# Kernel optimization log

Hardware: AMD Instinct MI355X
Metric: run time of the kernel (lower is better)

## Reference

```python
import jax, jax.numpy as jnp
import numpy as np
from jax.scipy.special import logsumexp

B, L, S, C = 8, 2048, 2048, 256
ITERS = 20

def setup_inputs() -> dict:
    key = jax.random.key(0)
    k0, k1 = jax.random.split(key)
    feat_c0 = jax.random.normal(k0, (B, L, C), dtype=jnp.float32)
    feat_c1 = jax.random.normal(k1, (B, S, C), dtype=jnp.float32)
    bin_score = jnp.ones((), dtype=jnp.float32)  # init_bin_score = 1.0
    return {"feat_c0": feat_c0, "feat_c1": feat_c1, "bin_score": bin_score}

def _uniform_prior(b, m, n):
    # build_uniform_prior: norm = -log(m+n); log_mu/[log_nu] over augmented rows/cols
    fm, fn = jnp.float32(m), jnp.float32(n)
    norm = -jnp.log(fm + fn)
    log_mu = jnp.concatenate([jnp.full((m,), norm, jnp.float32), (jnp.log(fn) + norm)[None]])
    log_nu = jnp.concatenate([jnp.full((n,), norm, jnp.float32), (jnp.log(fm) + norm)[None]])
    log_mu = jnp.broadcast_to(log_mu[None], (b, m + 1))
    log_nu = jnp.broadcast_to(log_nu[None], (b, n + 1))
    return log_mu, log_nu, norm

def _log_sinkhorn(Z, log_mu, log_nu, iters):
    u0 = jnp.zeros_like(log_mu)
    v0 = jnp.zeros_like(log_nu)
    def body(carry, _):
        u, v = carry
        u = log_mu - logsumexp(Z + v[:, None, :], axis=2)  # [B, M+1]
        v = log_nu - logsumexp(Z + u[:, :, None], axis=1)  # [B, N+1]
        return (u, v), None
    (u, v), _ = jax.lax.scan(body, (u0, v0), None, length=iters)
    return Z + u[:, :, None] + v[:, None, :]

def reference(feat_c0, feat_c1, bin_score):
    b, m, n = feat_c0.shape[0], feat_c0.shape[1], feat_c1.shape[1]
    scores = jnp.einsum('blc,bsc->bls', feat_c0, feat_c1)  # [B, M, N]
    # augment with dustbin row/col
    bins0 = jnp.broadcast_to(bin_score, (b, m, 1))
    bins1 = jnp.broadcast_to(bin_score, (b, 1, n))
    alpha = jnp.broadcast_to(bin_score, (b, 1, 1))
    Zin = jnp.concatenate([
        jnp.concatenate([scores, bins0], axis=-1),
        jnp.concatenate([bins1, alpha], axis=-1),
    ], axis=1)  # [B, M+1, N+1]
    log_mu, log_nu, norm = _uniform_prior(b, m, n)
    Z = _log_sinkhorn(Zin, log_mu, log_nu, ITERS)
    return Z - norm
```

## Files before the change

kernel.cpp:

```cpp
#include <hip/hip_runtime.h>

#define Bn 8
#define Mn 2048
#define Nn 2048
#define Cn 256
#define Np1 2049
#define Mp1 2049
#define UVS 2056
#define SINK_ITERS 20
#define NORM   (-8.3177661667193428f)
#define LOGBIN (-0.6931471805599453f)
#define LOG2E  (1.4426950408889634f)
#define LN2    (0.6931471805599453f)
#define NORM2  (-12.0f)
#define LOGBIN2 (-1.0f)
#define PNORM  (8.3177661667193428f)

#define EXP2(x) __builtin_amdgcn_exp2f(x)
#define LOG2(x) __builtin_amdgcn_logf(x)

typedef __bf16 v8bf __attribute__((ext_vector_type(8)));
typedef float  v4f  __attribute__((ext_vector_type(4)));
typedef unsigned short v8u __attribute__((ext_vector_type(8)));

__device__ __forceinline__ float bf2f(unsigned short h){
  return __uint_as_float(((unsigned)h) << 16);
}
__device__ __forceinline__ unsigned short f2bf(float f){
  unsigned u = __float_as_uint(f);
  return (unsigned short)((u + 0x7FFFu + ((u >> 16) & 1u)) >> 16);
}
__device__ __forceinline__ float ldS(const float* p){ return *p; }
__device__ __forceinline__ float ldS(const unsigned short* p){ return bf2f(*p); }
__device__ __forceinline__ void  stS(float* p, float x){ *p = x; }
__device__ __forceinline__ void  stS(unsigned short* p, float x){ *p = f2bf(x); }

__device__ __forceinline__ void ons(float x, float& m, float& s){
  if (x <= m) { s += __expf(x - m); }
  else        { s = s * __expf(m - x) + 1.0f; m = x; }
}
__device__ __forceinline__ void comb(float& m, float& s, float m2, float s2){
  if (m2 <= m) { s += s2 * __expf(m2 - m); }
  else         { s = s * __expf(m - m2) + s2; m = m2; }
}

__global__ void __launch_bounds__(256) conv_k(
    const float* __restrict__ in, unsigned short* __restrict__ out, float scale)
{
  size_t idx = (size_t)blockIdx.x * 256 + threadIdx.x;
  const float* p = in + idx * 8;
  v4f a = *(const v4f*)p;
  v4f c = *(const v4f*)(p + 4);
  v8u o;
  #pragma unroll
  for (int e = 0; e < 4; ++e){ o[e] = f2bf(a[e] * scale); o[e+4] = f2bf(c[e] * scale); }
  *(v8u*)(out + idx * 8) = o;
}

__global__ void __launch_bounds__(256) gemm_bt(
    const unsigned short* __restrict__ A, const unsigned short* __restrict__ Bm,
    unsigned short* __restrict__ S, unsigned short* __restrict__ ST)
{
  __shared__ unsigned short lt[4][64][65];
  int wid  = (blockIdx.x * 256 + threadIdx.x) >> 6;
  int w    = (threadIdx.x >> 6) & 3;
  int lane = threadIdx.x & 63;
  int b  = wid >> 10;
  int tt = wid & 1023;
  int i0 = (tt >> 5) << 6;
  int j0 = (tt & 31) << 6;
  int ln = lane & 15, qd = lane >> 4;
  const unsigned short* Ab = A  + (size_t)b * Mn * Cn;
  const unsigned short* Bb = Bm + (size_t)b * Nn * Cn;

  v4f acc[4][4];
  #pragma unroll
  for (int r = 0; r < 4; ++r)
    #pragma unroll
    for (int c = 0; c < 4; ++c)
      #pragma unroll
      for (int e = 0; e < 4; ++e) acc[r][c][e] = 0.0f;

  #pragma unroll
  for (int k0 = 0; k0 < Cn; k0 += 32){
    int kk = k0 + qd * 8;
    v8bf af[4], bfr[4];
    #pragma unroll
    for (int r = 0; r < 4; ++r)
      af[r] = *(const v8bf*)(const void*)(Ab + (size_t)(i0 + r*16 + ln) * Cn + kk);
    #pragma unroll
    for (int c = 0; c < 4; ++c)
      bfr[c] = *(const v8bf*)(const void*)(Bb + (size_t)(j0 + c*16 + ln) * Cn + kk);
    #pragma unroll
    for (int r = 0; r < 4; ++r)
      #pragma unroll
      for (int c = 0; c < 4; ++c)
        acc[r][c] = __builtin_amdgcn_mfma_f32_16x16x32_bf16(af[r], bfr[c], acc[r][c], 0, 0, 0);
  }

  unsigned short* Sb = S + (size_t)b * Mn * Nn;
  #pragma unroll
  for (int r = 0; r < 4; ++r){
    #pragma unroll
    for (int e = 0; e < 4; ++e){
      int lr = r*16 + qd*4 + e;
      #pragma unroll
      for (int c = 0; c < 4; ++c){
        unsigned short hv = f2bf(acc[r][c][e] * LOG2E);
        Sb[(size_t)(i0 + lr) * Nn + (j0 + c*16 + ln)] = hv;
        lt[w][lr][c*16 + ln] = hv;
      }
    }
  }
  unsigned short* Tb = ST + (size_t)b * Mn * Nn;
  #pragma unroll
  for (int r = 0; r < 4; ++r){
    #pragma unroll
    for (int e = 0; e < 4; ++e){
      int p = r*16 + qd*4 + e;
      #pragma unroll
      for (int c = 0; c < 4; ++c){
        int q = c*16 + ln;
        Tb[(size_t)(j0 + p) * Mn + (i0 + q)] = lt[w][q][p];
      }
    }
  }
}

__global__ void __launch_bounds__(256) rmax_k(
    const unsigned short* __restrict__ S, float* __restrict__ rmax)
{
  int b = blockIdx.y, lane = threadIdx.x & 63;
  int i = blockIdx.x * 4 + (threadIdx.x >> 6);
  const unsigned short* Sr = S + ((size_t)b * Mn + i) * Nn;
  float m = -3.0e38f;
  #pragma unroll
  for (int q = 0; q < 4; ++q){
    v8u sv = *(const v8u*)(Sr + q * 512 + lane * 8);
    #pragma unroll
    for (int c = 0; c < 8; ++c) m = fmaxf(m, bf2f(sv[c]));
  }
  #pragma unroll
  for (int off = 32; off > 0; off >>= 1) m = fmaxf(m, __shfl_xor(m, off));
  if (lane == 0) rmax[(size_t)b * UVS + i] = m;
}

__global__ void __launch_bounds__(256) pass4_k(
    const unsigned short* __restrict__ S, const float* __restrict__ vin,
    float* __restrict__ uout, const float* __restrict__ rmax,
    const float* __restrict__ binp)
{
  int b = blockIdx.y, t = threadIdx.x;
  const float* vb = vin + (size_t)b * UVS;
  __shared__ float red[8];
  if (blockIdx.x < Mn / 8){
    int lane = t & 63, wv = t >> 6;
    int i0 = blockIdx.x * 8 + wv * 2;
    v4f va[8];
    #pragma unroll
    for (int q = 0; q < 4; ++q){
      int j0 = q * 512 + lane * 8;
      va[2*q]   = *(const v4f*)(vb + j0);
      va[2*q+1] = *(const v4f*)(vb + j0 + 4);
    }
    float mv = va[0][0];
    #pragma unroll
    for (int h = 0; h < 8; ++h)
      #pragma unroll
      for (int e = 0; e < 4; ++e) mv = fmaxf(mv, va[h][e]);
    #pragma unroll
    for (int off = 32; off > 0; off >>= 1) mv = fmaxf(mv, __shfl_xor(mv, off));
    float bin2 = binp[0] * LOG2E;
    float vN  = vb[Nn];
    float bvn = bin2 + vN;
    float sh0 = fmaxf(rmax[(size_t)b * UVS + i0]     + mv, bvn);
    float sh1 = fmaxf(rmax[(size_t)b * UVS + i0 + 1] + mv, bvn);
    const unsigned short* Sr0 = S + ((size_t)b * Mn + i0) * Nn;
    const unsigned short* Sr1 = Sr0 + Nn;
    float a0=0.f,a1=0.f,a2=0.f,a3=0.f;
    float c0=0.f,c1=0.f,c2=0.f,c3=0.f;
    #pragma unroll
    for (int q = 0; q < 4; ++q){
      int j0 = q * 512 + lane * 8;
      v8u r0 = *(const v8u*)(Sr0 + j0);
      v8u r1 = *(const v8u*)(Sr1 + j0);
      a0 += EXP2(bf2f(r0[0]) + va[2*q][0]   - sh0);
      a1 += EXP2(bf2f(r0[1]) + va[2*q][1]   - sh0);
      a2 += EXP2(bf2f(r0[2]) + va[2*q][2]   - sh0);
      a3 += EXP2(bf2f(r0[3]) + va[2*q][3]   - sh0);
      c0 += EXP2(bf2f(r1[0]) + va[2*q][0]   - sh1);
      c1 += EXP2(bf2f(r1[1]) + va[2*q][1]   - sh1);
      c2 += EXP2(bf2f(r1[2]) + va[2*q][2]   - sh1);
      c3 += EXP2(bf2f(r1[3]) + va[2*q][3]   - sh1);
      a0 += EXP2(bf2f(r0[4]) + va[2*q+1][0] - sh0);
      a1 += EXP2(bf2f(r0[5]) + va[2*q+1][1] - sh0);
      a2 += EXP2(bf2f(r0[6]) + va[2*q+1][2] - sh0);
      a3 += EXP2(bf2f(r0[7]) + va[2*q+1][3] - sh0);
      c0 += EXP2(bf2f(r1[4]) + va[2*q+1][0] - sh1);
      c1 += EXP2(bf2f(r1[5]) + va[2*q+1][1] - sh1);
      c2 += EXP2(bf2f(r1[6]) + va[2*q+1][2] - sh1);
      c3 += EXP2(bf2f(r1[7]) + va[2*q+1][3] - sh1);
    }
    float sA = (a0 + a1) + (a2 + a3);
    float sB = (c0 + c1) + (c2 + c3);
    #pragma unroll
    for (int off = 32; off > 0; off >>= 1){
      sA += __shfl_xor(sA, off);
      sB += __shfl_xor(sB, off);
    }
    if (lane == 0){
      sA += EXP2(bvn - sh0);
      sB += EXP2(bvn - sh1);
      uout[(size_t)b * UVS + i0]     = NORM2 - (sh0 + LOG2(sA));
      uout[(size_t)b * UVS + i0 + 1] = NORM2 - (sh1 + LOG2(sB));
    }
  } else {
    float x[9];
    #pragma unroll
    for (int k = 0; k < 9; ++k){
      int j = t + k * 256;
      x[k] = (j <= Nn) ? vb[j] : -3.0e38f;
    }
    float m = x[0];
    #pragma unroll
    for (int k = 1; k < 9; ++k) m = fmaxf(m, x[k]);
    #pragma unroll
    for (int off = 32; off > 0; off >>= 1) m = fmaxf(m, __shfl_down(m, off));
    int w = t >> 6;
    if ((t & 63) == 0) red[w] = m;
    __syncthreads();
    float M = fmaxf(fmaxf(red[0], red[1]), fmaxf(red[2], red[3]));
    float s = 0.0f;
    #pragma unroll
    for (int k = 0; k < 9; ++k) s += EXP2(x[k] - M);
    #pragma unroll
    for (int off = 32; off > 0; off >>= 1) s += __shfl_down(s, off);
    __syncthreads();
    if ((t & 63) == 0) red[w] = s;
    __syncthreads();
    if (t == 0){
      float Ss = red[0] + red[1] + red[2] + red[3];
      float bin2 = binp[0] * LOG2E;
      uout[(size_t)b * UVS + Mn] = LOGBIN2 - (bin2 + M + LOG2(Ss));
    }
  }
}

__global__ void __launch_bounds__(256) final2_k(
    const unsigned short* __restrict__ S, float* __restrict__ out,
    const float* __restrict__ u, const float* __restrict__ v,
    const float* __restrict__ binp)
{
  int i = blockIdx.x, b = blockIdx.y, t = threadIdx.x;
  float bin2 = binp[0] * LOG2E;
  const float* vb = v + (size_t)b * UVS;
  float ui = u[(size_t)b * UVS + i];
  float* ob = out + ((size_t)b * Mp1 + i) * Np1;
  if (i < Mn){
    const unsigned short* Sr = S + ((size_t)b * Mn + i) * Nn;
    int j0 = t * 8;
    v8u sv = *(const v8u*)(Sr + j0);
    v4f va = *(const v4f*)(vb + j0);
    v4f vc = *(const v4f*)(vb + j0 + 4);
    #pragma unroll
    for (int c = 0; c < 4; ++c) ob[j0 + c]     = (bf2f(sv[c])   + ui + va[c]) * LN2 + PNORM;
    #pragma unroll
    for (int c = 0; c < 4; ++c) ob[j0 + 4 + c] = (bf2f(sv[c+4]) + ui + vc[c]) * LN2 + PNORM;
    if (t == 0) ob[Nn] = (bin2 + ui + vb[Nn]) * LN2 + PNORM;
  } else {
    for (int j = t; j <= Nn; j += 256) ob[j] = (bin2 + ui + vb[j]) * LN2 + PNORM;
  }
}

template<typename ST>
__global__ void __launch_bounds__(256) gemm_k(
    const float* __restrict__ A, const float* __restrict__ Bm,
    ST* __restrict__ S, long srow, long sbatch)
{
  int wid  = (blockIdx.x * 256 + threadIdx.x) >> 6;
  int lane = threadIdx.x & 63;
  int b  = wid >> 10;
  int tt = wid & 1023;
  int i0 = (tt >> 5) << 6;
  int j0 = (tt & 31) << 6;
  int ln = lane & 15, qd = lane >> 4;
  const float* Ab = A  + (size_t)b * Mn * Cn;
  const float* Bb = Bm + (size_t)b * Nn * Cn;

  v4f acc[4][4];
  #pragma unroll
  for (int r = 0; r < 4; ++r)
    #pragma unroll
    for (int c = 0; c < 4; ++c)
      #pragma unroll
      for (int e = 0; e < 4; ++e) acc[r][c][e] = 0.0f;

  #pragma unroll
  for (int k0 = 0; k0 < Cn; k0 += 32){
    int kk = k0 + qd * 8;
    v8bf af[4], bfr[4];
    #pragma unroll
    for (int r = 0; r < 4; ++r){
      const float* p = Ab + (size_t)(i0 + r*16 + ln) * Cn + kk;
      v4f lo = *(const v4f*)p, hi = *(const v4f*)(p + 4);
      #pragma unroll
      for (int e = 0; e < 4; ++e){ af[r][e] = (__bf16)lo[e]; af[r][e+4] = (__bf16)hi[e]; }
    }
    #pragma unroll
    for (int c = 0; c < 4; ++c){
      const float* p = Bb + (size_t)(j0 + c*16 + ln) * Cn + kk;
      v4f lo = *(const v4f*)p, hi = *(const v4f*)(p + 4);
      #pragma unroll
      for (int e = 0; e < 4; ++e){ bfr[c][e] = (__bf16)lo[e]; bfr[c][e+4] = (__bf16)hi[e]; }
    }
    #pragma unroll
    for (int r = 0; r < 4; ++r)
      #pragma unroll
      for (int c = 0; c < 4; ++c)
        acc[r][c] = __builtin_amdgcn_mfma_f32_16x16x32_bf16(af[r], bfr[c], acc[r][c], 0, 0, 0);
  }

  ST* Sb = S + (size_t)b * sbatch;
  #pragma unroll
  for (int r = 0; r < 4; ++r){
    #pragma unroll
    for (int e = 0; e < 4; ++e){
      int row = i0 + r*16 + qd*4 + e;
      #pragma unroll
      for (int c = 0; c < 4; ++c)
        stS(Sb + (size_t)row * srow + (j0 + c*16 + ln), acc[r][c][e]);
    }
  }
}

__global__ void __launch_bounds__(256) row_pass_t(
    const unsigned short* __restrict__ S, const float* __restrict__ vin,
    float* __restrict__ uout, const float* __restrict__ binp)
{
  int b = blockIdx.y, t = threadIdx.x;
  const float* vb = vin + (size_t)b * UVS;
  __shared__ float red[8];
  if (blockIdx.x < Mn / 4){
    int lane = t & 63;
    int i = blockIdx.x * 4 + (t >> 6);
    const unsigned short* Sr = S + ((size_t)b * Mn + i) * Nn;
    float x[32];
    #pragma unroll
    for (int q = 0; q < 4; ++q){
      int j0 = q * 512 + lane * 8;
      v8u sv = *(const v8u*)(Sr + j0);
      v4f va = *(const v4f*)(vb + j0);
      v4f vc = *(const v4f*)(vb + j0 + 4);
      #pragma unroll
      for (int c = 0; c < 4; ++c){
        x[q*8 + c]     = bf2f(sv[c])   + va[c];
        x[q*8 + 4 + c] = bf2f(sv[c+4]) + vc[c];
      }
    }
    float mx[16];
    #pragma unroll
    for (int k = 0; k < 16; ++k) mx[k] = fmaxf(x[2*k], x[2*k+1]);
    #pragma unroll
    for (int k = 0; k < 8; ++k) mx[k] = fmaxf(mx[k], mx[k+8]);
    #pragma unroll
    for (int k = 0; k < 4; ++k) mx[k] = fmaxf(mx[k], mx[k+4]);
    float m = fmaxf(fmaxf(mx[0], mx[1]), fmaxf(mx[2], mx[3]));
    #pragma unroll
    for (int off = 32; off > 0; off >>= 1) m = fmaxf(m, __shfl_xor(m, off));
    float s0 = 0.f, s1 = 0.f, s2 = 0.f, s3 = 0.f;
    #pragma unroll
    for (int k = 0; k < 8; ++k){
      s0 += __expf(x[4*k]     - m);
      s1 += __expf(x[4*k + 1] - m);
      s2 += __expf(x[4*k + 2] - m);
      s3 += __expf(x[4*k + 3] - m);
    }
    float s = (s0 + s1) + (s2 + s3);
    #pragma unroll
    for (int off = 32; off > 0; off >>= 1) s += __shfl_xor(s, off);
    if (lane == 0){
      float M = m, Ss = s;
      comb(M, Ss, binp[0] + vb[Nn], 1.0f);
      uout[(size_t)b * UVS + i] = NORM - (M + __logf(Ss));
    }
  } else {
    float x[9];
    #pragma unroll
    for (int k = 0; k < 9; ++k){
      int j = t + k * 256;
      x[k] = (j <= Nn) ? vb[j] : -3.0e38f;
    }
    float m = x[0];
    #pragma unroll
    for (int k = 1; k < 9; ++k) m = fmaxf(m, x[k]);
    #pragma unroll
    for (int off = 32; off > 0; off >>= 1) m = fmaxf(m, __shfl_down(m, off));
    int w = t >> 6;
    if ((t & 63) == 0) red[w] = m;
    __syncthreads();
    float M = fmaxf(fmaxf(red[0], red[1]), fmaxf(red[2], red[3]));
    float s = 0.0f;
    #pragma unroll
    for (int k = 0; k < 9; ++k) s += __expf(x[k] - M);
    #pragma unroll
    for (int off = 32; off > 0; off >>= 1) s += __shfl_down(s, off);
    __syncthreads();
    if ((t & 63) == 0) red[w] = s;
    __syncthreads();
    if (t == 0){
      float Ss = red[0] + red[1] + red[2] + red[3];
      uout[(size_t)b * UVS + Mn] = LOGBIN - (binp[0] + M + __logf(Ss));
    }
  }
}

__global__ void __launch_bounds__(256) row_pass_v(
    const unsigned short* __restrict__ S, const float* __restrict__ v,
    float* __restrict__ u, const float* __restrict__ binp)
{
  int i = blockIdx.x, b = blockIdx.y, t = threadIdx.x;
  const float* vb = v + (size_t)b * UVS;
  float x[9];
  int K;
  if (i < Mn){
    const unsigned short* Sr = S + ((size_t)b * Mn + i) * Nn;
    int j0 = t * 8;
    v8u sv = *(const v8u*)(Sr + j0);
    v4f va = *(const v4f*)(vb + j0);
    v4f vc = *(const v4f*)(vb + j0 + 4);
    #pragma unroll
    for (int c = 0; c < 4; ++c){ x[c] = bf2f(sv[c]) + va[c]; x[c+4] = bf2f(sv[c+4]) + vc[c]; }
    K = 8;
  } else {
    #pragma unroll
    for (int k = 0; k < 9; ++k){
      int j = t + k * 256;
      x[k] = (j <= Nn) ? vb[j] : -3.0e38f;
    }
    K = 9;
  }
  float m = x[0];
  #pragma unroll
  for (int k = 1; k < 9; ++k) if (k < K) m = fmaxf(m, x[k]);
  #pragma unroll
  for (int off = 32; off > 0; off >>= 1) m = fmaxf(m, __shfl_down(m, off));
  __shared__ float red[8];
  int w = t >> 6;
  if ((t & 63) == 0) red[w] = m;
  __syncthreads();
  float M = fmaxf(fmaxf(red[0], red[1]), fmaxf(red[2], red[3]));
  float s = 0.0f;
  #pragma unroll
  for (int k = 0; k < 9; ++k) if (k < K) s += __expf(x[k] - M);
  #pragma unroll
  for (int off = 32; off > 0; off >>= 1) s += __shfl_down(s, off);
  __syncthreads();
  if ((t & 63) == 0) red[w] = s;
  __syncthreads();
  if (t == 0){
    float Ss = red[0] + red[1] + red[2] + red[3];
    float bin = binp[0];
    if (i < Mn){
      comb(M, Ss, bin + vb[Nn], 1.0f);
      u[(size_t)b * UVS + i] = NORM - (M + __logf(Ss));
    } else {
      u[(size_t)b * UVS + Mn] = LOGBIN - (bin + M + __logf(Ss));
    }
  }
}

__global__ void __launch_bounds__(256) col_pass_v(
    const unsigned short* __restrict__ S, const float* __restrict__ u,
    float* __restrict__ v, const float* __restrict__ binp)
{
  int blk = blockIdx.x, b = blockIdx.y, t = threadIdx.x;
  const float* ub = u + (size_t)b * UVS;
  __shared__ float lm[32][65];
  __shared__ float ls[32][65];
  __shared__ float red[16];
  if (blk < Nn / 64){
    int tx = t & 7, ty = t >> 3;
    int j0 = blk * 64 + tx * 8;
    const unsigned short* Sb = S + (size_t)b * Mn * Nn;
    float m[8], s[8];
    #pragma unroll
    for (int c = 0; c < 8; ++c){ m[c] = -3.0e38f; s[c] = 0.0f; }
    for (int i = ty; i < Mn; i += 32){
      v8u sv = *(const v8u*)(Sb + (size_t)i * Nn + j0);
      float ui = ub[i];
      #pragma unroll
      for (int c = 0; c < 8; ++c){
        float x  = bf2f(sv[c]) + ui;
        float mn = fmaxf(m[c], x);
        s[c] = s[c] * __expf(m[c] - mn) + __expf(x - mn);
        m[c] = mn;
      }
    }
    #pragma unroll
    for (int c = 0; c < 8; ++c){ lm[ty][tx*8 + c] = m[c]; ls[ty][tx*8 + c] = s[c]; }
    __syncthreads();
    if (t < 64){
      float M = -3.0e38f, Ss = 0.0f;
      #pragma unroll 4
      for (int rg = 0; rg < 32; ++rg) comb(M, Ss, lm[rg][t], ls[rg][t]);
      float bin = binp[0];
      comb(M, Ss, bin + ub[Mn], 1.0f);
      v[(size_t)b * UVS + blk * 64 + t] = NORM - (M + __logf(Ss));
    }
  } else {
    float x[9];
    #pragma unroll
    for (int k = 0; k < 9; ++k){
      int j = t + k * 256;
      x[k] = (j <= Mn) ? ub[j] : -3.0e38f;
    }
    float m = x[0];
    #pragma unroll
    for (int k = 1; k < 9; ++k) m = fmaxf(m, x[k]);
    #pragma unroll
    for (int off = 32; off > 0; off >>= 1) m = fmaxf(m, __shfl_down(m, off));
    int w = t >> 6;
    if ((t & 63) == 0) red[w] = m;
    __syncthreads();
    float M = fmaxf(fmaxf(red[0], red[1]), fmaxf(red[2], red[3]));
    float s = 0.0f;
    #pragma unroll
    for (int k = 0; k < 9; ++k) s += __expf(x[k] - M);
    #pragma unroll
    for (int off = 32; off > 0; off >>= 1) s += __shfl_down(s, off);
    __syncthreads();
    if ((t & 63) == 0) red[w] = s;
    __syncthreads();
    if (t == 0){
      float Ss = red[0] + red[1] + red[2] + red[3];
      float bin = binp[0];
      v[(size_t)b * UVS + Nn] = LOGBIN - (bin + M + __logf(Ss));
    }
  }
}

__global__ void __launch_bounds__(256) final_v(
    const unsigned short* __restrict__ S, float* __restrict__ out,
    const float* __restrict__ u, const float* __restrict__ v,
    const float* __restrict__ binp)
{
  int i = blockIdx.x, b = blockIdx.y, t = threadIdx.x;
  float bin = binp[0];
  const float* vb = v + (size_t)b * UVS;
  float ui = u[(size_t)b * UVS + i];
  float* ob = out + ((size_t)b * Mp1 + i) * Np1;
  if (i < Mn){
    const unsigned short* Sr = S + ((size_t)b * Mn + i) * Nn;
    int j0 = t * 8;
    v8u sv = *(const v8u*)(Sr + j0);
    v4f va = *(const v4f*)(vb + j0);
    v4f vc = *(const v4f*)(vb + j0 + 4);
    #pragma unroll
    for (int c = 0; c < 4; ++c) ob[j0 + c]     = bf2f(sv[c])   + ui + va[c] - NORM;
    #pragma unroll
    for (int c = 0; c < 4; ++c) ob[j0 + 4 + c] = bf2f(sv[c+4]) + ui + vc[c] - NORM;
    if (t == 0) ob[Nn] = bin + ui + vb[Nn] - NORM;
  } else {
    for (int j = t; j <= Nn; j += 256) ob[j] = bin + ui + vb[j] - NORM;
  }
}

template<typename ST>
__global__ void __launch_bounds__(256) row_pass(
    const ST* __restrict__ S, long srow, long sbatch,
    const float* __restrict__ v, float* __restrict__ u,
    const float* __restrict__ binp)
{
  int i = blockIdx.x, b = blockIdx.y, t = threadIdx.x;
  const float* vb = v + (size_t)b * UVS;
  float m = -3.0e38f, s = 0.0f;
  if (i < Mn){
    const ST* Sr = S + (size_t)b * sbatch + (size_t)i * srow;
    #pragma unroll
    for (int jj = 0; jj < Nn / 256; ++jj){
      int j = jj * 256 + t;
      ons(ldS(Sr + j) + vb[j], m, s);
    }
  } else {
    for (int j = t; j <= Nn; j += 256) ons(vb[j], m, s);
  }
  #pragma unroll
  for (int off = 32; off > 0; off >>= 1){
    float m2 = __shfl_down(m, off);
    float s2 = __shfl_down(s, off);
    comb(m, s, m2, s2);
  }
  __shared__ float sm[4], ss[4];
  int w = t >> 6;
  if ((t & 63) == 0){ sm[w] = m; ss[w] = s; }
  __syncthreads();
  if (t == 0){
    #pragma unroll
    for (int w2 = 1; w2 < 4; ++w2) comb(m, s, sm[w2], ss[w2]);
    float bin = binp[0];
    if (i < Mn){
      comb(m, s, bin + vb[Nn], 1.0f);
      u[(size_t)b * UVS + i] = NORM - (m + __logf(s));
    } else {
      u[(size_t)b * UVS + Mn] = LOGBIN - (bin + m + __logf(s));
    }
  }
}

template<typename ST>
__global__ void __launch_bounds__(1024) col_pass(
    const ST* __restrict__ S, long srow, long sbatch,
    const float* __restrict__ u, float* __restrict__ v,
    const float* __restrict__ binp)
{
  int jt = blockIdx.x, b = blockIdx.y, t = threadIdx.x;
  const float* ub = u + (size_t)b * UVS;
  __shared__ float sm[16][64];
  __shared__ float ss[16][64];
  if (jt < Nn / 64){
    int c = t & 63, rg = t >> 6;
    int j = jt * 64 + c;
    const ST* Sc = S + (size_t)b * sbatch + j;
    float m = -3.0e38f, s = 0.0f;
    #pragma unroll 8
    for (int i = rg; i < Mn; i += 16)
      ons(ldS(Sc + (size_t)i * srow) + ub[i], m, s);
    sm[rg][c] = m; ss[rg][c] = s;
    __syncthreads();
    if (rg == 0){
      #pragma unroll
      for (int r = 1; r < 16; ++r) comb(m, s, sm[r][c], ss[r][c]);
      float bin = binp[0];
      comb(m, s, bin + ub[Mn], 1.0f);
      v[(size_t)b * UVS + j] = NORM - (m + __logf(s));
    }
  } else {
    float m = -3.0e38f, s = 0.0f;
    for (int i = t; i <= Mn; i += 1024) ons(ub[i], m, s);
    #pragma unroll
    for (int off = 32; off > 0; off >>= 1){
      float m2 = __shfl_down(m, off);
      float s2 = __shfl_down(s, off);
      comb(m, s, m2, s2);
    }
    int w = t >> 6;
    if ((t & 63) == 0){ sm[0][w] = m; ss[0][w] = s; }
    __syncthreads();
    if (t == 0){
      #pragma unroll
      for (int w2 = 1; w2 < 16; ++w2) comb(m, s, sm[0][w2], ss[0][w2]);
      float bin = binp[0];
      v[(size_t)b * UVS + Nn] = LOGBIN - (bin + m + __logf(s));
    }
  }
}

template<typename ST>
__global__ void __launch_bounds__(256) final_k(
    const ST* __restrict__ S, long srow, long sbatch,
    float* __restrict__ out, const float* __restrict__ u,
    const float* __restrict__ v, const float* __restrict__ binp)
{
  int i = blockIdx.x, b = blockIdx.y, t = threadIdx.x;
  float bin = binp[0];
  float ui = u[(size_t)b * UVS + i];
  const float* vb = v + (size_t)b * UVS;
  float* ob = out + ((size_t)b * Mp1 + i) * Np1;
  if (i < Mn){
    const ST* Sr = S + (size_t)b * sbatch + (size_t)i * srow;
    for (int j = t; j < Nn; j += 256)
      ob[j] = ldS(Sr + j) + ui + vb[j] - NORM;
    if (t == 0) ob[Nn] = bin + ui + vb[Nn] - NORM;
  } else {
    for (int j = t; j <= Nn; j += 256)
      ob[j] = bin + ui + vb[j] - NORM;
  }
}

__global__ void zero_uv(float* uv){
  int t = blockIdx.x * 256 + threadIdx.x;
  if (t < 2 * Bn * UVS) uv[t] = 0.0f;
}

extern "C" void kernel_launch(void* const* d_in, const int* in_sizes, int n_in,
                              void* d_out, int out_size, void* d_ws, size_t ws_size,
                              hipStream_t stream)
{
  const float* A    = (const float*)d_in[0];
  const float* Bm   = (const float*)d_in[1];
  const float* binp = (const float*)d_in[2];
  float* out = (float*)d_out;

  const size_t S_bytes  = (size_t)Bn * Mn * Nn * 2;
  const size_t AB_bytes = (size_t)Bn * Mn * Cn * 2;
  const size_t uv_bytes = (size_t)4 * Bn * UVS * 4;
  bool useT2 = ws_size >= 2 * S_bytes + 2 * AB_bytes + uv_bytes;
  bool useT  = ws_size >= 2 * S_bytes + 2 * (size_t)Bn * UVS * 4;
  bool useW  = ws_size >= S_bytes + 2 * (size_t)Bn * UVS * 4;

  float* u;
  unsigned short* Sw  = nullptr;
  unsigned short* STw = nullptr;
  unsigned short* Abf = nullptr;
  unsigned short* Bbf = nullptr;
  if (useT2){
    Sw  = (unsigned short*)d_ws;
    STw = (unsigned short*)((char*)d_ws + S_bytes);
    Abf = (unsigned short*)((char*)d_ws + 2 * S_bytes);
    Bbf = (unsigned short*)((char*)d_ws + 2 * S_bytes + AB_bytes);
    u   = (float*)((char*)d_ws + 2 * S_bytes + 2 * AB_bytes);
  } else if (useT){
    Sw  = (unsigned short*)d_ws;
    STw = (unsigned short*)((char*)d_ws + S_bytes);
    u   = (float*)((char*)d_ws + 2 * S_bytes);
  } else if (useW){
    Sw = (unsigned short*)d_ws;
    u  = (float*)((char*)d_ws + S_bytes);
  } else {
    u  = (float*)d_ws;
  }
  float* v = u + (size_t)Bn * UVS;

  zero_uv<<<(2 * Bn * UVS + 255) / 256, 256, 0, stream>>>(u);

  if (useT2){
    float* rmaxS = v + (size_t)Bn * UVS;
    float* rmaxT = rmaxS + (size_t)Bn * UVS;
    const int cgrid = (Bn * Mn * Cn / 8) / 256;
    conv_k<<<cgrid, 256, 0, stream>>>(A,  Abf, 1.0f);
    conv_k<<<cgrid, 256, 0, stream>>>(Bm, Bbf, 1.0f);
    gemm_bt<<<(Bn * 32 * 32) / 4, 256, 0, stream>>>(Abf, Bbf, Sw, STw);
    rmax_k<<<dim3(Mn / 4, Bn), 256, 0, stream>>>(Sw,  rmaxS);
    rmax_k<<<dim3(Nn / 4, Bn), 256, 0, stream>>>(STw, rmaxT);
    for (int it = 0; it < SINK_ITERS; ++it){
      pass4_k<<<dim3(Mn / 8 + 1, Bn), 256, 0, stream>>>(Sw,  v, u, rmaxS, binp);
      pass4_k<<<dim3(Nn / 8 + 1, Bn), 256, 0, stream>>>(STw, u, v, rmaxT, binp);
    }
    final2_k<<<dim3(Mp1, Bn), 256, 0, stream>>>(Sw, out, u, v, binp);
  } else if (useT){
    gemm_k<unsigned short><<<(Bn * 32 * 32) / 4, 256, 0, stream>>>(A, Bm, Sw,  Nn, (long)Mn * Nn);
    gemm_k<unsigned short><<<(Bn * 32 * 32) / 4, 256, 0, stream>>>(Bm, A, STw, Mn, (long)Mn * Nn);
    for (int it = 0; it < SINK_ITERS; ++it){
      row_pass_t<<<dim3(Mn / 4 + 1, Bn), 256, 0, stream>>>(Sw,  v, u, binp);
      row_pass_t<<<dim3(Nn / 4 + 1, Bn), 256, 0, stream>>>(STw, u, v, binp);
    }
    final_v<<<dim3(Mp1, Bn), 256, 0, stream>>>(Sw, out, u, v, binp);
  } else if (useW){
    gemm_k<unsigned short><<<(Bn * 32 * 32) / 4, 256, 0, stream>>>(A, Bm, Sw, Nn, (long)Mn * Nn);
    for (int it = 0; it < SINK_ITERS; ++it){
      row_pass_v<<<dim3(Mp1, Bn), 256, 0, stream>>>(Sw, v, u, binp);
      col_pass_v<<<dim3(Nn / 64 + 1, Bn), 256, 0, stream>>>(Sw, u, v, binp);
    }
    final_v<<<dim3(Mp1, Bn), 256, 0, stream>>>(Sw, out, u, v, binp);
  } else {
    const long srow = Np1, sbatch = (long)Mp1 * Np1;
    gemm_k<float><<<(Bn * 32 * 32) / 4, 256, 0, stream>>>(A, Bm, out, srow, sbatch);
    for (int it = 0; it < SINK_ITERS; ++it){
      row_pass<float><<<dim3(Mp1, Bn), 256, 0, stream>>>(out, srow, sbatch, v, u, binp);
      col_pass<float><<<dim3(Nn / 64 + 1, Bn), 1024, 0, stream>>>(out, srow, sbatch, u, v, binp);
    }
    final_k<float><<<dim3(Mp1, Bn), 256, 0, stream>>>(out, srow, sbatch, out, u, v, binp);
  }
}
```

Before: 745.3 us.

## Fuse row/column max computation into GEMM epilogue via atomicMax; nontemporal loads

Removes the two rmax_k passes that re-read S and ST after the GEMM. Row and column maxima are now computed from the fp32 accumulators in the GEMM epilogue and merged across tiles with atomicMax on order-preserving unsigned keys. The pass4 kernel also uses nontemporal loads for the score rows. The zeroing kernel grows to clear the max buffers, at the cost of extra shuffles and atomics in the GEMM. The maxima now come from fp32 values scaled by LOG2E rather than bf16-rounded values, so the shift differs slightly from the stored data.

```diff
diff --git a/kernel.cpp b/kernel.cpp
--- a/kernel.cpp
+++ b/kernel.cpp
@@ -35,6 +35,15 @@
 __device__ __forceinline__ void  stS(float* p, float x){ *p = x; }
 __device__ __forceinline__ void  stS(unsigned short* p, float x){ *p = f2bf(x); }
 
+__device__ __forceinline__ unsigned fkey(float x){
+  unsigned u = __float_as_uint(x);
+  return (u & 0x80000000u) ? ~u : (u | 0x80000000u);
+}
+__device__ __forceinline__ float fdec(unsigned k){
+  unsigned u = (k & 0x80000000u) ? (k ^ 0x80000000u) : ~k;
+  return __uint_as_float(u);
+}
+
 __device__ __forceinline__ void ons(float x, float& m, float& s){
   if (x <= m) { s += __expf(x - m); }
   else        { s = s * __expf(m - x) + 1.0f; m = x; }
@@ -59,7 +68,8 @@
 
 __global__ void __launch_bounds__(256) gemm_bt(
     const unsigned short* __restrict__ A, const unsigned short* __restrict__ Bm,
-    unsigned short* __restrict__ S, unsigned short* __restrict__ ST)
+    unsigned short* __restrict__ S, unsigned short* __restrict__ ST,
+    unsigned* __restrict__ rmS, unsigned* __restrict__ rmT)
 {
   __shared__ unsigned short lt[4][64][65];
   int wid  = (blockIdx.x * 256 + threadIdx.x) >> 6;
@@ -125,29 +135,38 @@
       }
     }
   }
-}
-
-__global__ void __launch_bounds__(256) rmax_k(
-    const unsigned short* __restrict__ S, float* __restrict__ rmax)
-{
-  int b = blockIdx.y, lane = threadIdx.x & 63;
-  int i = blockIdx.x * 4 + (threadIdx.x >> 6);
-  const unsigned short* Sr = S + ((size_t)b * Mn + i) * Nn;
-  float m = -3.0e38f;
-  #pragma unroll
-  for (int q = 0; q < 4; ++q){
-    v8u sv = *(const v8u*)(Sr + q * 512 + lane * 8);
-    #pragma unroll
-    for (int c = 0; c < 8; ++c) m = fmaxf(m, bf2f(sv[c]));
-  }
-  #pragma unroll
-  for (int off = 32; off > 0; off >>= 1) m = fmaxf(m, __shfl_xor(m, off));
-  if (lane == 0) rmax[(size_t)b * UVS + i] = m;
+  unsigned* rS = rmS + (size_t)b * UVS;
+  #pragma unroll
+  for (int r = 0; r < 4; ++r){
+    #pragma unroll
+    for (int e = 0; e < 4; ++e){
+      float m = fmaxf(fmaxf(acc[r][0][e], acc[r][1][e]), fmaxf(acc[r][2][e], acc[r][3][e]));
+      m *= LOG2E;
+      m = fmaxf(m, __shfl_xor(m, 1));
+      m = fmaxf(m, __shfl_xor(m, 2));
+      m = fmaxf(m, __shfl_xor(m, 4));
+      m = fmaxf(m, __shfl_xor(m, 8));
+      if (ln == 0) atomicMax(rS + (i0 + r*16 + qd*4 + e), fkey(m));
+    }
+  }
+  unsigned* rT = rmT + (size_t)b * UVS;
+  #pragma unroll
+  for (int c = 0; c < 4; ++c){
+    float m = -3.0e38f;
+    #pragma unroll
+    for (int r = 0; r < 4; ++r)
+      #pragma unroll
+      for (int e = 0; e < 4; ++e) m = fmaxf(m, acc[r][c][e]);
+    m *= LOG2E;
+    m = fmaxf(m, __shfl_xor(m, 16));
+    m = fmaxf(m, __shfl_xor(m, 32));
+    if (qd == 0) atomicMax(rT + (j0 + c*16 + ln), fkey(m));
+  }
 }
 
 __global__ void __launch_bounds__(256) pass4_k(
     const unsigned short* __restrict__ S, const float* __restrict__ vin,
-    float* __restrict__ uout, const float* __restrict__ rmax,
+    float* __restrict__ uout, const unsigned* __restrict__ rmax,
     const float* __restrict__ binp)
 {
   int b = blockIdx.y, t = threadIdx.x;
@@ -173,8 +192,8 @@
     float bin2 = binp[0] * LOG2E;
     float vN  = vb[Nn];
     float bvn = bin2 + vN;
-    float sh0 = fmaxf(rmax[(size_t)b * UVS + i0]     + mv, bvn);
-    float sh1 = fmaxf(rmax[(size_t)b * UVS + i0 + 1] + mv, bvn);
+    float sh0 = fmaxf(fdec(rmax[(size_t)b * UVS + i0])     + mv, bvn);
+    float sh1 = fmaxf(fdec(rmax[(size_t)b * UVS + i0 + 1]) + mv, bvn);
     const unsigned short* Sr0 = S + ((size_t)b * Mn + i0) * Nn;
     const unsigned short* Sr1 = Sr0 + Nn;
     float a0=0.f,a1=0.f,a2=0.f,a3=0.f;
@@ -182,8 +201,8 @@
     #pragma unroll
     for (int q = 0; q < 4; ++q){
       int j0 = q * 512 + lane * 8;
-      v8u r0 = *(const v8u*)(Sr0 + j0);
-      v8u r1 = *(const v8u*)(Sr1 + j0);
+      v8u r0 = __builtin_nontemporal_load((const v8u*)(Sr0 + j0));
+      v8u r1 = __builtin_nontemporal_load((const v8u*)(Sr1 + j0));
       a0 += EXP2(bf2f(r0[0]) + va[2*q][0]   - sh0);
       a1 += EXP2(bf2f(r0[1]) + va[2*q][1]   - sh0);
       a2 += EXP2(bf2f(r0[2]) + va[2*q][2]   - sh0);
@@ -414,6 +433,32 @@
   }
 }
 
+__global__ void __launch_bounds__(256) final_v(
+    const unsigned short* __restrict__ S, float* __restrict__ out,
+    const float* __restrict__ u, const float* __restrict__ v,
+    const float* __restrict__ binp)
+{
+  int i = blockIdx.x, b = blockIdx.y, t = threadIdx.x;
+  float bin = binp[0];
+  const float* vb = v + (size_t)b * UVS;
+  float ui = u[(size_t)b * UVS + i];
+  float* ob = out + ((size_t)b * Mp1 + i) * Np1;
+  if (i < Mn){
+    const unsigned short* Sr = S + ((size_t)b * Mn + i) * Nn;
+    int j0 = t * 8;
+    v8u sv = *(const v8u*)(Sr + j0);
+    v4f va = *(const v4f*)(vb + j0);
+    v4f vc = *(const v4f*)(vb + j0 + 4);
+    #pragma unroll
+    for (int c = 0; c < 4; ++c) ob[j0 + c]     = bf2f(sv[c])   + ui + va[c] - NORM;
+    #pragma unroll
+    for (int c = 0; c < 4; ++c) ob[j0 + 4 + c] = bf2f(sv[c+4]) + ui + vc[c] - NORM;
+    if (t == 0) ob[Nn] = bin + ui + vb[Nn] - NORM;
+  } else {
+    for (int j = t; j <= Nn; j += 256) ob[j] = bin + ui + vb[j] - NORM;
+  }
+}
+
 __global__ void __launch_bounds__(256) row_pass_v(
     const unsigned short* __restrict__ S, const float* __restrict__ v,
     float* __restrict__ u, const float* __restrict__ binp)
@@ -536,32 +581,6 @@
       float bin = binp[0];
       v[(size_t)b * UVS + Nn] = LOGBIN - (bin + M + __logf(Ss));
     }
-  }
-}
-
-__global__ void __launch_bounds__(256) final_v(
-    const unsigned short* __restrict__ S, float* __restrict__ out,
-    const float* __restrict__ u, const float* __restrict__ v,
-    const float* __restrict__ binp)
-{
-  int i = blockIdx.x, b = blockIdx.y, t = threadIdx.x;
-  float bin = binp[0];
-  const float* vb = v + (size_t)b * UVS;
-  float ui = u[(size_t)b * UVS + i];
-  float* ob = out + ((size_t)b * Mp1 + i) * Np1;
-  if (i < Mn){
-    const unsigned short* Sr = S + ((size_t)b * Mn + i) * Nn;
-    int j0 = t * 8;
-    v8u sv = *(const v8u*)(Sr + j0);
-    v4f va = *(const v4f*)(vb + j0);
-    v4f vc = *(const v4f*)(vb + j0 + 4);
-    #pragma unroll
-    for (int c = 0; c < 4; ++c) ob[j0 + c]     = bf2f(sv[c])   + ui + va[c] - NORM;
-    #pragma unroll
-    for (int c = 0; c < 4; ++c) ob[j0 + 4 + c] = bf2f(sv[c+4]) + ui + vc[c] - NORM;
-    if (t == 0) ob[Nn] = bin + ui + vb[Nn] - NORM;
-  } else {
-    for (int j = t; j <= Nn; j += 256) ob[j] = bin + ui + vb[j] - NORM;
   }
 }
 
@@ -679,7 +698,7 @@
 
 __global__ void zero_uv(float* uv){
   int t = blockIdx.x * 256 + threadIdx.x;
-  if (t < 2 * Bn * UVS) uv[t] = 0.0f;
+  if (t < 4 * Bn * UVS + 64) uv[t] = 0.0f;
 }
 
 extern "C" void kernel_launch(void* const* d_in, const int* in_sizes, int n_in,
@@ -693,7 +712,7 @@
 
   const size_t S_bytes  = (size_t)Bn * Mn * Nn * 2;
   const size_t AB_bytes = (size_t)Bn * Mn * Cn * 2;
-  const size_t uv_bytes = (size_t)4 * Bn * UVS * 4;
+  const size_t uv_bytes = (size_t)4 * Bn * UVS * 4 + 256;
   bool useT2 = ws_size >= 2 * S_bytes + 2 * AB_bytes + uv_bytes;
   bool useT  = ws_size >= 2 * S_bytes + 2 * (size_t)Bn * UVS * 4;
   bool useW  = ws_size >= S_bytes + 2 * (size_t)Bn * UVS * 4;
@@ -721,17 +740,15 @@
   }
   float* v = u + (size_t)Bn * UVS;
 
-  zero_uv<<<(2 * Bn * UVS + 255) / 256, 256, 0, stream>>>(u);
+  zero_uv<<<(4 * Bn * UVS + 64 + 255) / 256, 256, 0, stream>>>(u);
 
   if (useT2){
-    float* rmaxS = v + (size_t)Bn * UVS;
-    float* rmaxT = rmaxS + (size_t)Bn * UVS;
+    unsigned* rmaxS = (unsigned*)(v + (size_t)Bn * UVS);
+    unsigned* rmaxT = rmaxS + (size_t)Bn * UVS;
     const int cgrid = (Bn * Mn * Cn / 8) / 256;
     conv_k<<<cgrid, 256, 0, stream>>>(A,  Abf, 1.0f);
     conv_k<<<cgrid, 256, 0, stream>>>(Bm, Bbf, 1.0f);
-    gemm_bt<<<(Bn * 32 * 32) / 4, 256, 0, stream>>>(Abf, Bbf, Sw, STw);
-    rmax_k<<<dim3(Mn / 4, Bn), 256, 0, stream>>>(Sw,  rmaxS);
-    rmax_k<<<dim3(Nn / 4, Bn), 256, 0, stream>>>(STw, rmaxT);
+    gemm_bt<<<(Bn * 32 * 32) / 4, 256, 0, stream>>>(Abf, Bbf, Sw, STw, rmaxS, rmaxT);
     for (int it = 0; it < SINK_ITERS; ++it){
       pass4_k<<<dim3(Mn / 8 + 1, Bn), 256, 0, stream>>>(Sw,  v, u, rmaxS, binp);
       pass4_k<<<dim3(Nn / 8 + 1, Bn), 256, 0, stream>>>(STw, u, v, rmaxT, binp);
```

Result: slower. 782.8 us (+5.0%).
